# Kernel optimization log

Hardware: AMD Instinct MI355X
Metric: run time of the kernel (lower is better)

## Reference

```python
import jax, jax.numpy as jnp
import numpy as np

HEADS, BS, HALO = 8, 8, 3
WIN = BS + 2 * HALO  # 14


def setup_inputs() -> dict:
    key = jax.random.key(0)
    k1, k2, k3, k4 = jax.random.split(key, 4)
    B, C, H, W = 16, 256, 64, 64
    dim_out_qk, dim_out_v = 256, 256
    std = C ** (-0.5)
    x = jax.random.normal(k1, (B, C, H, W), jnp.float32)
    Wq = jax.random.normal(k2, (dim_out_qk, C), jnp.float32) * std
    Wkv = jax.random.normal(k3, (dim_out_qk + dim_out_v, C), jnp.float32) * std
    pos_bias = jax.random.normal(k4, (HEADS, BS * BS, WIN * WIN), jnp.float32) * 0.02
    return {"x": x, "Wq": Wq, "Wkv": Wkv, "pos_bias": pos_bias}


def reference(x, Wq, Wkv, pos_bias):
    B, C, H, W = x.shape
    dhqk = Wq.shape[0] // HEADS            # 32
    dhv = Wkv.shape[0] // HEADS - dhqk     # 32
    scale = dhqk ** (-0.5)
    nhb, nwb = H // BS, W // BS
    nb = nhb * nwb

    xl = jnp.transpose(x, (0, 2, 3, 1))    # [B, H, W, C]

    # queries: [B, heads, nb, bs^2, dhqk] (row-major within block)
    q = xl @ Wq.T
    q = q.reshape(B, nhb, BS, nwb, BS, HEADS, dhqk)
    q = q.transpose(0, 5, 1, 3, 2, 4, 6).reshape(B, HEADS, nb, BS * BS, dhqk)

    # keys/values via overlapping halo windows (zero-padded unfold)
    kv = xl @ Wkv.T                                       # [B, H, W, dim_kv]
    kv = jnp.pad(kv, ((0, 0), (HALO, HALO), (HALO, HALO), (0, 0)))
    ridx = (jnp.arange(nhb) * BS)[:, None] + jnp.arange(WIN)[None, :]
    cidx = (jnp.arange(nwb) * BS)[:, None] + jnp.arange(WIN)[None, :]
    kv = kv[:, ridx]
    kv = kv[:, :, :, cidx]
    kv = kv.transpose(0, 1, 3, 2, 4, 5).reshape(B, nb, WIN * WIN, HEADS, dhqk + dhv)
    k = kv[..., :dhqk]
    v = kv[..., dhqk:]

    attn = jnp.einsum('bhnqd,bnkhd->bhnqk', q, k) * scale + pos_bias[None, :, None]
    attn = jax.nn.softmax(attn, axis=-1)
    out = jnp.einsum('bhnqk,bnkhd->bhnqd', attn, v)       # [B, heads, nb, bs^2, dhv]

    out = out.reshape(B, HEADS, nhb, nwb, BS, BS, dhv)
    out = out.transpose(0, 1, 6, 2, 4, 3, 5).reshape(B, HEADS * dhv, H, W)
    return out
```

## Files before the change

kernel.cpp:

```cpp
#include <hip/hip_runtime.h>
#include <hip/hip_bf16.h>
#include <stdint.h>

#define HEADS 8
#define WIN 14
#define NPOS 196
#define NPAD 224
#define NB 16
#define NC 256
#define NH 64
#define NW 64
#define NP 4096
#define NKV 512
#define NOC 768

typedef __bf16 bf16_t;
typedef bf16_t bf16x8 __attribute__((ext_vector_type(8)));
typedef float f32x4 __attribute__((ext_vector_type(4)));

union Frag {
  uint4 u4;
  bf16x8 b8;
  ushort us[8];
};

__device__ __forceinline__ ushort f2bf(float f) {
  bf16_t h = (bf16_t)f;
  return __builtin_bit_cast(ushort, h);
}
__device__ __forceinline__ bf16x8 load_bf8(const float* __restrict__ p) {
  float4 a = *reinterpret_cast<const float4*>(p);
  float4 b = *reinterpret_cast<const float4*>(p + 4);
  bf16x8 r;
  r[0] = (bf16_t)a.x; r[1] = (bf16_t)a.y; r[2] = (bf16_t)a.z; r[3] = (bf16_t)a.w;
  r[4] = (bf16_t)b.x; r[5] = (bf16_t)b.y; r[6] = (bf16_t)b.z; r[7] = (bf16_t)b.w;
  return r;
}

__device__ ushort g_wb[NOC * NC];

__global__ __launch_bounds__(256) void k_wcast(const float* __restrict__ wq,
                                               const float* __restrict__ wkv) {
  int idx = (blockIdx.x * 256 + threadIdx.x) * 8;
  int oc = idx >> 8, c = idx & 255;
  const float* src = (oc < 256) ? (wq + (size_t)oc * NC + c)
                                : (wkv + (size_t)(oc - 256) * NC + c);
  Frag v;
  v.b8 = load_bf8(src);
  *reinterpret_cast<uint4*>(g_wb + idx) = v.u4;
}

__global__ __launch_bounds__(256) void k_xt(const float* __restrict__ x,
                                            ushort* __restrict__ xt) {
  __shared__ __align__(16) ushort ls[64][66];
  const int b = blockIdx.z, p0 = blockIdx.x * 64, c0 = blockIdx.y * 64;
  const int tid = threadIdx.x;
  #pragma unroll
  for (int it = 0; it < 4; ++it) {
    int i = it * 256 + tid;
    int c = i >> 4, ps = (i & 15) * 4;
    float4 v = *reinterpret_cast<const float4*>(x + ((size_t)(b * NC + c0 + c)) * NP + p0 + ps);
    ls[ps + 0][c] = f2bf(v.x);
    ls[ps + 1][c] = f2bf(v.y);
    ls[ps + 2][c] = f2bf(v.z);
    ls[ps + 3][c] = f2bf(v.w);
  }
  __syncthreads();
  #pragma unroll
  for (int it = 0; it < 2; ++it) {
    int i = it * 256 + tid;
    int p = i >> 3, cs = (i & 7) * 8;
    Frag o;
    #pragma unroll
    for (int j = 0; j < 8; ++j) o.us[j] = ls[p][cs + j];
    *reinterpret_cast<uint4*>(xt + ((size_t)(b * NP) + p0 + p) * NC + c0 + cs) = o.u4;
  }
}

__global__ __launch_bounds__(256, 2) void k_proj2(const ushort* __restrict__ xt,
                                                  ushort* __restrict__ qkv) {
  __shared__ __align__(16) ushort As[128][264];
  const int row0 = blockIdx.x * 128;
  const int n0 = blockIdx.y * 256;
  const int tid = threadIdx.x, lane = tid & 63, wid = tid >> 6;
  const int quad = lane >> 4, lc = lane & 15;
  #pragma unroll
  for (int it = 0; it < 16; ++it) {
    int i = it * 256 + tid;
    int r = i >> 5, cs = (i & 31) * 8;
    uint4 v = *reinterpret_cast<const uint4*>(xt + ((size_t)(row0 + r)) * NC + cs);
    *reinterpret_cast<uint4*>(&As[r][cs]) = v;
  }
  __syncthreads();
  const int wm = (wid & 1) * 64, wn = (wid >> 1) * 128;
  f32x4 acc[4][8] = {};
  #pragma unroll
  for (int ks = 0; ks < 8; ++ks) {
    const int k0 = ks * 32 + quad * 8;
    Frag a[4];
    #pragma unroll
    for (int mt = 0; mt < 4; ++mt)
      a[mt].u4 = *reinterpret_cast<const uint4*>(&As[wm + mt * 16 + lc][k0]);
    #pragma unroll
    for (int ng = 0; ng < 2; ++ng) {
      Frag bb[4];
      #pragma unroll
      for (int j = 0; j < 4; ++j) {
        int oc = n0 + wn + (ng * 4 + j) * 16 + lc;
        bb[j].u4 = *reinterpret_cast<const uint4*>(g_wb + (size_t)oc * NC + k0);
      }
      #pragma unroll
      for (int mt = 0; mt < 4; ++mt)
        #pragma unroll
        for (int j = 0; j < 4; ++j)
          acc[mt][ng * 4 + j] = __builtin_amdgcn_mfma_f32_16x16x32_bf16(
              a[mt].b8, bb[j].b8, acc[mt][ng * 4 + j], 0, 0, 0);
    }
  }
  __syncthreads();
  #pragma unroll
  for (int mt = 0; mt < 4; ++mt)
    #pragma unroll
    for (int nn = 0; nn < 8; ++nn)
      #pragma unroll
      for (int r = 0; r < 4; ++r)
        As[wm + mt * 16 + quad * 4 + r][wn + nn * 16 + lc] = f2bf(acc[mt][nn][r]);
  __syncthreads();
  #pragma unroll
  for (int it = 0; it < 16; ++it) {
    int i = it * 256 + tid;
    int r = i >> 5, cs = (i & 31) * 8;
    uint4 u = *reinterpret_cast<const uint4*>(&As[r][cs]);
    *reinterpret_cast<uint4*>(qkv + ((size_t)(row0 + r)) * NOC + n0 + cs) = u;
  }
}

__global__ __launch_bounds__(256) void k_attn_f2(const ushort* __restrict__ qkv,
                                                 const float* __restrict__ pbias,
                                                 float* __restrict__ out) {
  __shared__ __align__(16) ushort ksh[NPAD][40];
  __shared__ __align__(16) ushort vth[32][232];
  __shared__ __align__(16) ushort psh[4][16][32];
  float (*osh)[33] = reinterpret_cast<float(*)[33]>(&ksh[0][0]);
  const int b = blockIdx.z, h = blockIdx.y, blk = blockIdx.x;
  const int by = blk >> 3, bx = blk & 7;
  const int tid = threadIdx.x, lane = tid & 63, w = tid >> 6;
  const int quad = lane >> 4, lc = lane & 15;

  Frag aq;
  {
    int q = w * 16 + lc;
    int py = by * 8 + (q >> 3), px = bx * 8 + (q & 7);
    aq.u4 = *reinterpret_cast<const uint4*>(
        qkv + ((size_t)(b * NP + py * NW + px)) * NOC + h * 32 + quad * 8);
  }

  for (int it = 0; it < 7; ++it) {
    int i = it * 256 + tid;
    int pos = i >> 3, seg = i & 7;
    Frag v;
    v.u4 = make_uint4(0u, 0u, 0u, 0u);
    if (pos < NPOS) {
      int wy = pos / WIN;
      int wx = pos - wy * WIN;
      int yq = by * 8 - 3 + wy, xx = bx * 8 - 3 + wx;
      if ((unsigned)yq < (unsigned)NH && (unsigned)xx < (unsigned)NW)
        v.u4 = *reinterpret_cast<const uint4*>(
            qkv + ((size_t)(b * NP + yq * NW + xx)) * NOC + 256 + h * 64 + seg * 8);
    }
    if (seg < 4) {
      *reinterpret_cast<uint4*>(&ksh[pos][seg * 8]) = v.u4;
    } else {
      int d0 = (seg - 4) * 8;
      int cp = pos ^ ((seg - 4) << 3);
      #pragma unroll
      for (int j = 0; j < 8; ++j) vth[d0 + j][cp] = v.us[j];
    }
  }
  __syncthreads();

  f32x4 s[14];
  #pragma unroll
  for (int nt = 0; nt < 14; ++nt) {
    Frag bk;
    bk.u4 = *reinterpret_cast<const uint4*>(&ksh[nt * 16 + lc][quad * 8]);
    f32x4 z = {0.f, 0.f, 0.f, 0.f};
    s[nt] = __builtin_amdgcn_mfma_f32_16x16x32_bf16(aq.b8, bk.b8, z, 0, 0, 0);
  }

  const float scale = 0.17677669529663687f;
  const int qi = w * 16 + quad * 4;
  float lsum[4] = {0.f, 0.f, 0.f, 0.f};
  #pragma unroll
  for (int nt = 0; nt < 14; ++nt) {
    int col = nt * 16 + lc;
    #pragma unroll
    for (int r = 0; r < 4; ++r) {
      float p = 0.f;
      if (col < NPOS)
        p = __expf(s[nt][r] * scale + pbias[(size_t)(h * 64 + qi + r) * NPOS + col]);
      s[nt][r] = p;
      lsum[r] += p;
    }
  }

  f32x4 o[2] = {};
  #pragma unroll
  for (int kt = 0; kt < 7; ++kt) {
    #pragma unroll
    for (int t = 0; t < 2; ++t)
      #pragma unroll
      for (int r = 0; r < 4; ++r)
        psh[w][quad * 4 + r][t * 16 + lc] = f2bf(s[2 * kt + t][r]);
    Frag ap;
    ap.u4 = *reinterpret_cast<const uint4*>(&psh[w][lc][quad * 8]);
    #pragma unroll
    for (int t = 0; t < 2; ++t) {
      int d = t * 16 + lc;
      int g = (kt * 4 + quad) ^ ((d >> 3) & 3);
      Frag bv;
      bv.u4 = *reinterpret_cast<const uint4*>(&vth[d][g * 8]);
      o[t] = __builtin_amdgcn_mfma_f32_16x16x32_bf16(ap.b8, bv.b8, o[t], 0, 0, 0);
    }
  }

  #pragma unroll
  for (int m = 1; m < 16; m <<= 1)
    #pragma unroll
    for (int r = 0; r < 4; ++r) lsum[r] += __shfl_xor(lsum[r], m);
  float rinv[4];
  #pragma unroll
  for (int r = 0; r < 4; ++r) rinv[r] = 1.0f / lsum[r];

  __syncthreads();
  #pragma unroll
  for (int t = 0; t < 2; ++t)
    #pragma unroll
    for (int r = 0; r < 4; ++r)
      osh[w * 16 + quad * 4 + r][t * 16 + lc] = o[t][r] * rinv[r];
  __syncthreads();

  {
    int d = tid >> 3, yy = tid & 7;
    float4 o0, o1;
    o0.x = osh[yy * 8 + 0][d]; o0.y = osh[yy * 8 + 1][d];
    o0.z = osh[yy * 8 + 2][d]; o0.w = osh[yy * 8 + 3][d];
    o1.x = osh[yy * 8 + 4][d]; o1.y = osh[yy * 8 + 5][d];
    o1.z = osh[yy * 8 + 6][d]; o1.w = osh[yy * 8 + 7][d];
    float* op = out + ((size_t)(b * NC + h * 32 + d) * NH + by * 8 + yy) * NW + bx * 8;
    *reinterpret_cast<float4*>(op) = o0;
    *reinterpret_cast<float4*>(op + 4) = o1;
  }
}

__global__ __launch_bounds__(256) void k_proj_r4(const float* __restrict__ x,
                                                 const float* __restrict__ wq,
                                                 const float* __restrict__ wkv,
                                                 ushort* __restrict__ qkv) {
  __shared__ __align__(16) ushort As[64][264];
  const int b = blockIdx.z, y = blockIdx.x;
  const int n0 = blockIdx.y * 256;
  const int tid = threadIdx.x, lane = tid & 63, wid = tid >> 6;
  const int quad = lane >> 4, lc = lane & 15;
  #pragma unroll
  for (int it = 0; it < 16; ++it) {
    int i = it * 256 + tid;
    int c = i >> 4, xs = (i & 15) * 4;
    float4 v = *reinterpret_cast<const float4*>(x + ((size_t)(b * NC + c)) * NP + y * NW + xs);
    #pragma unroll
    for (int j = 0; j < 4; ++j) {
      int row = xs + j;
      float f = (j == 0) ? v.x : (j == 1) ? v.y : (j == 2) ? v.z : v.w;
      As[row][c ^ ((((row >> 2) & 3)) << 3)] = f2bf(f);
    }
  }
  __syncthreads();
  const int wm = (wid & 1) * 32, wn = (wid >> 1) * 128;
  const int swz = ((lc >> 2) & 3) << 3;
  f32x4 acc[2][8] = {};
  #pragma unroll
  for (int ks = 0; ks < 8; ++ks) {
    const int k0 = ks * 32 + quad * 8;
    Frag a0, a1;
    a0.u4 = *reinterpret_cast<const uint4*>(&As[wm + lc][k0 ^ swz]);
    a1.u4 = *reinterpret_cast<const uint4*>(&As[wm + 16 + lc][k0 ^ swz]);
    #pragma unroll
    for (int nh = 0; nh < 2; ++nh) {
      bf16x8 bb[4];
      #pragma unroll
      for (int nt = 0; nt < 4; ++nt) {
        int oc = n0 + wn + nh * 64 + nt * 16 + lc;
        const float* wp = (oc < 256) ? (wq + (size_t)oc * NC) : (wkv + (size_t)(oc - 256) * NC);
        bb[nt] = load_bf8(wp + k0);
      }
      #pragma unroll
      for (int nt = 0; nt < 4; ++nt) {
        acc[0][nh * 4 + nt] = __builtin_amdgcn_mfma_f32_16x16x32_bf16(a0.b8, bb[nt], acc[0][nh * 4 + nt], 0, 0, 0);
        acc[1][nh * 4 + nt] = __builtin_amdgcn_mfma_f32_16x16x32_bf16(a1.b8, bb[nt], acc[1][nh * 4 + nt], 0, 0, 0);
      }
    }
  }
  __syncthreads();
  #pragma unroll
  for (int mt = 0; mt < 2; ++mt)
    #pragma unroll
    for (int nn = 0; nn < 8; ++nn)
      #pragma unroll
      for (int r = 0; r < 4; ++r)
        As[wm + mt * 16 + quad * 4 + r][wn + nn * 16 + lc] = f2bf(acc[mt][nn][r]);
  __syncthreads();
  #pragma unroll
  for (int v8 = 0; v8 < 8; ++v8) {
    int flat = v8 * 256 + tid;
    int p = flat >> 5, seg = flat & 31;
    uint4 u = *reinterpret_cast<const uint4*>(&As[p][seg * 8]);
    *reinterpret_cast<uint4*>(qkv + ((size_t)(b * NP) + y * NW + p) * NOC + n0 + seg * 8) = u;
  }
}

__global__ __launch_bounds__(256) void k_kv(const float* __restrict__ x,
                                            const float* __restrict__ wkv,
                                            ushort* __restrict__ kvb) {
  __shared__ __align__(16) ushort As[64][264];
  const int b = blockIdx.z;
  const int y = blockIdx.x;
  const int n0 = blockIdx.y * 128;
  const int tid = threadIdx.x;
  const int lane = tid & 63, wid = tid >> 6;
  const int quad = lane >> 4, lc = lane & 15;
  #pragma unroll
  for (int it = 0; it < 16; ++it) {
    int i = it * 256 + tid;
    int c = i >> 4, xs = (i & 15) * 4;
    float4 v = *reinterpret_cast<const float4*>(x + ((size_t)(b * NC + c)) * NP + y * NW + xs);
    As[xs + 0][c] = f2bf(v.x);
    As[xs + 1][c] = f2bf(v.y);
    As[xs + 2][c] = f2bf(v.z);
    As[xs + 3][c] = f2bf(v.w);
  }
  __syncthreads();
  const int wm = (wid & 1) * 32, wn = (wid >> 1) * 64;
  f32x4 acc[2][4] = {};
  #pragma unroll
  for (int ks = 0; ks < 8; ++ks) {
    const int k0 = ks * 32 + quad * 8;
    Frag a[2];
    bf16x8 bb[4];
    #pragma unroll
    for (int mt = 0; mt < 2; ++mt)
      a[mt].u4 = *reinterpret_cast<const uint4*>(&As[wm + mt * 16 + lc][k0]);
    #pragma unroll
    for (int nt = 0; nt < 4; ++nt) {
      int oc = n0 + wn + nt * 16 + lc;
      bb[nt] = load_bf8(wkv + (size_t)oc * NC + k0);
    }
    #pragma unroll
    for (int mt = 0; mt < 2; ++mt)
      #pragma unroll
      for (int nt = 0; nt < 4; ++nt)
        acc[mt][nt] = __builtin_amdgcn_mfma_f32_16x16x32_bf16(a[mt].b8, bb[nt], acc[mt][nt], 0, 0, 0);
  }
  #pragma unroll
  for (int mt = 0; mt < 2; ++mt) {
    #pragma unroll
    for (int r = 0; r < 4; ++r) {
      int pl = wm + mt * 16 + quad * 4 + r;
      #pragma unroll
      for (int nt = 0; nt < 4; ++nt) {
        int oc = n0 + wn + nt * 16 + lc;
        kvb[((size_t)(b * NP + y * NW + pl)) * NKV + oc] = f2bf(acc[mt][nt][r]);
      }
    }
  }
}

__global__ __launch_bounds__(256) void k_attn_v3(const float* __restrict__ x,
                                                 const float* __restrict__ wq,
                                                 const ushort* __restrict__ kvb,
                                                 const float* __restrict__ pbias,
                                                 float* __restrict__ out) {
  __shared__ __align__(16) ushort ksh[NPAD][40];
  __shared__ __align__(16) ushort vth[32][232];
  __shared__ __align__(16) ushort psh[4][16][232];
  __shared__ __align__(16) ushort qsh[4][16][32];
  __shared__ __align__(16) float osh[64][33];
  const int b = blockIdx.z, h = blockIdx.y, blk = blockIdx.x;
  const int by = blk >> 3, bx = blk & 7;
  const int tid = threadIdx.x, lane = tid & 63, w = tid >> 6;
  const int quad = lane >> 4, lc = lane & 15;

  for (int it = 0; it < 7; ++it) {
    int i = it * 256 + tid;
    int pos = i >> 3, seg = i & 7;
    Frag v;
    v.u4 = make_uint4(0u, 0u, 0u, 0u);
    if (pos < NPOS) {
      int wy = pos / WIN;
      int wx = pos - wy * WIN;
      int yq = by * 8 - 3 + wy, xx = bx * 8 - 3 + wx;
      if ((unsigned)yq < (unsigned)NH && (unsigned)xx < (unsigned)NW)
        v.u4 = *reinterpret_cast<const uint4*>(
            kvb + ((size_t)(b * NP + yq * NW + xx)) * NKV + h * 64 + seg * 8);
    }
    if (seg < 4) {
      *reinterpret_cast<uint4*>(&ksh[pos][seg * 8]) = v.u4;
    } else {
      int d0 = (seg - 4) * 8;
      #pragma unroll
      for (int j = 0; j < 8; ++j) vth[d0 + j][pos] = v.us[j];
    }
  }

  f32x4 qacc[2] = {};
  {
    const int q = w * 16 + lc;
    const size_t p = (size_t)(by * 8 + (q >> 3)) * NW + bx * 8 + (q & 7);
    #pragma unroll
    for (int ks = 0; ks < 8; ++ks) {
      const int k0 = ks * 32 + quad * 8;
      Frag ax;
      #pragma unroll
      for (int j = 0; j < 8; ++j)
        ax.us[j] = f2bf(x[((size_t)(b * NC + k0 + j)) * NP + p]);
      bf16x8 bw0 = load_bf8(wq + (size_t)(h * 32 + lc) * NC + k0);
      bf16x8 bw1 = load_bf8(wq + (size_t)(h * 32 + 16 + lc) * NC + k0);
      qacc[0] = __builtin_amdgcn_mfma_f32_16x16x32_bf16(ax.b8, bw0, qacc[0], 0, 0, 0);
      qacc[1] = __builtin_amdgcn_mfma_f32_16x16x32_bf16(ax.b8, bw1, qacc[1], 0, 0, 0);
    }
  }
  #pragma unroll
  for (int t = 0; t < 2; ++t)
    #pragma unroll
    for (int r = 0; r < 4; ++r)
      qsh[w][quad * 4 + r][t * 16 + lc] = f2bf(qacc[t][r]);
  Frag aq;
  aq.u4 = *reinterpret_cast<const uint4*>(&qsh[w][lc][quad * 8]);

  __syncthreads();

  f32x4 s[14];
  #pragma unroll
  for (int nt = 0; nt < 14; ++nt) {
    Frag bk;
    bk.u4 = *reinterpret_cast<const uint4*>(&ksh[nt * 16 + lc][quad * 8]);
    f32x4 z = {0.f, 0.f, 0.f, 0.f};
    s[nt] = __builtin_amdgcn_mfma_f32_16x16x32_bf16(aq.b8, bk.b8, z, 0, 0, 0);
  }

  const float scale = 0.17677669529663687f;
  const int qi = w * 16 + quad * 4;
  float lsum[4] = {0.f, 0.f, 0.f, 0.f};
  #pragma unroll
  for (int nt = 0; nt < 14; ++nt) {
    int col = nt * 16 + lc;
    #pragma unroll
    for (int r = 0; r < 4; ++r) {
      float p = 0.f;
      if (col < NPOS)
        p = __expf(s[nt][r] * scale + pbias[(size_t)(h * 64 + qi + r) * NPOS + col]);
      s[nt][r] = p;
      lsum[r] += p;
    }
  }
  #pragma unroll
  for (int m = 1; m < 16; m <<= 1) {
    #pragma unroll
    for (int r = 0; r < 4; ++r) lsum[r] += __shfl_xor(lsum[r], m);
  }
  #pragma unroll
  for (int nt = 0; nt < 14; ++nt) {
    #pragma unroll
    for (int r = 0; r < 4; ++r) psh[w][quad * 4 + r][nt * 16 + lc] = f2bf(s[nt][r]);
  }
  f32x4 o[2] = {};
  #pragma unroll
  for (int kt = 0; kt < 7; ++kt) {
    Frag ap;
    ap.u4 = *reinterpret_cast<const uint4*>(&psh[w][lc][kt * 32 + quad * 8]);
    #pragma unroll
    for (int t = 0; t < 2; ++t) {
      Frag bv;
      bv.u4 = *reinterpret_cast<const uint4*>(&vth[t * 16 + lc][kt * 32 + quad * 8]);
      o[t] = __builtin_amdgcn_mfma_f32_16x16x32_bf16(ap.b8, bv.b8, o[t], 0, 0, 0);
    }
  }
  #pragma unroll
  for (int t = 0; t < 2; ++t)
    #pragma unroll
    for (int r = 0; r < 4; ++r)
      osh[w * 16 + quad * 4 + r][t * 16 + lc] = o[t][r] / lsum[r];
  __syncthreads();
  {
    int d = tid >> 3, yy = tid & 7;
    float4 o0, o1;
    o0.x = osh[yy * 8 + 0][d]; o0.y = osh[yy * 8 + 1][d];
    o0.z = osh[yy * 8 + 2][d]; o0.w = osh[yy * 8 + 3][d];
    o1.x = osh[yy * 8 + 4][d]; o1.y = osh[yy * 8 + 5][d];
    o1.z = osh[yy * 8 + 6][d]; o1.w = osh[yy * 8 + 7][d];
    float* op = out + ((size_t)(b * NC + h * 32 + d) * NH + by * 8 + yy) * NW + bx * 8;
    *reinterpret_cast<float4*>(op) = o0;
    *reinterpret_cast<float4*>(op + 4) = o1;
  }
}

extern "C" void kernel_launch(void* const* d_in, const int* in_sizes, int n_in,
                              void* d_out, int out_size, void* d_ws, size_t ws_size,
                              hipStream_t stream) {
  const float* x   = (const float*)d_in[0];
  const float* wq  = (const float*)d_in[1];
  const float* wkv = (const float*)d_in[2];
  const float* pb  = (const float*)d_in[3];
  float* outp = (float*)d_out;

  const size_t qkv_bytes = (size_t)NB * NP * NOC * sizeof(ushort);
  const size_t xt_bytes  = (size_t)NB * NP * NC * sizeof(ushort);

  if (ws_size >= qkv_bytes + xt_bytes) {
    ushort* qkv = (ushort*)d_ws;
    ushort* xt  = (ushort*)((char*)d_ws + qkv_bytes);
    k_wcast<<<dim3(NOC * NC / (256 * 8)), 256, 0, stream>>>(wq, wkv);
    k_xt<<<dim3(NP / 64, NC / 64, NB), 256, 0, stream>>>(x, xt);
    k_proj2<<<dim3(NB * NP / 128, 3), 256, 0, stream>>>(xt, qkv);
    k_attn_f2<<<dim3(64, HEADS, NB), 256, 0, stream>>>(qkv, pb, outp);
  } else if (ws_size >= qkv_bytes) {
    ushort* qkv = (ushort*)d_ws;
    k_proj_r4<<<dim3(NH, 3, NB), 256, 0, stream>>>(x, wq, wkv, qkv);
    k_attn_f2<<<dim3(64, HEADS, NB), 256, 0, stream>>>(qkv, pb, outp);
  } else {
    ushort* kvb = (ushort*)d_ws;
    k_kv<<<dim3(NH, NKV / 128, NB), 256, 0, stream>>>(x, wkv, kvb);
    k_attn_v3<<<dim3(64, HEADS, NB), 256, 0, stream>>>(x, wq, kvb, pb, outp);
  }
}
```

Before: 291.4 us.

## Swizzle xt layout for direct global-to-LDS loads and pre-transpose position bias

k_xt now writes xt with an XOR-swizzled 8-element group order, so k_proj2 can copy its A tile straight into LDS with global_load_lds and read it back conflict-free through the same XOR swizzle. The padded LDS row is dropped, and the epilogue staging uses the swizzle too. A new k_pbt kernel transposes pos_bias once per call into a [head][key][query] layout padded with large negative values, so the attention kernel loads four biases with one float4 and no column bounds check. The cost is an extra small kernel launch and a tighter coupling of the xt layout between the two kernels.

```diff
diff --git a/kernel.cpp b/kernel.cpp
--- a/kernel.cpp
+++ b/kernel.cpp
@@ -37,7 +37,18 @@
   return r;
 }
 
+__device__ __forceinline__ void gload_lds16(const ushort* g, ushort* l) {
+#if __has_builtin(__builtin_amdgcn_global_load_lds)
+  __builtin_amdgcn_global_load_lds(
+      (const __attribute__((address_space(1))) unsigned int*)(const void*)g,
+      (__attribute__((address_space(3))) unsigned int*)(void*)l, 16, 0, 0);
+#else
+  *reinterpret_cast<uint4*>(l) = *reinterpret_cast<const uint4*>(g);
+#endif
+}
+
 __device__ ushort g_wb[NOC * NC];
+__device__ float g_pbt[HEADS * NPAD * 64];
 
 __global__ __launch_bounds__(256) void k_wcast(const float* __restrict__ wq,
                                                const float* __restrict__ wkv) {
@@ -50,10 +61,20 @@
   *reinterpret_cast<uint4*>(g_wb + idx) = v.u4;
 }
 
+__global__ __launch_bounds__(256) void k_pbt(const float* __restrict__ pb) {
+  const int h = blockIdx.y;
+  const int key = blockIdx.x * 4 + (threadIdx.x >> 6);
+  const int q = threadIdx.x & 63;
+  float v = -30000.0f;
+  if (key < NPOS) v = pb[((size_t)(h * 64 + q)) * NPOS + key];
+  g_pbt[((size_t)(h * NPAD) + key) * 64 + q] = v;
+}
+
 __global__ __launch_bounds__(256) void k_xt(const float* __restrict__ x,
                                             ushort* __restrict__ xt) {
   __shared__ __align__(16) ushort ls[64][66];
   const int b = blockIdx.z, p0 = blockIdx.x * 64, c0 = blockIdx.y * 64;
+  const int by8 = blockIdx.y * 8;
   const int tid = threadIdx.x;
   #pragma unroll
   for (int it = 0; it < 4; ++it) {
@@ -69,27 +90,27 @@
   #pragma unroll
   for (int it = 0; it < 2; ++it) {
     int i = it * 256 + tid;
-    int p = i >> 3, cs = (i & 7) * 8;
+    int p = i >> 3, gl = i & 7;
     Frag o;
     #pragma unroll
-    for (int j = 0; j < 8; ++j) o.us[j] = ls[p][cs + j];
-    *reinterpret_cast<uint4*>(xt + ((size_t)(b * NP) + p0 + p) * NC + c0 + cs) = o.u4;
+    for (int j = 0; j < 8; ++j) o.us[j] = ls[p][gl * 8 + j];
+    int gph = by8 + (gl ^ (p & 7));
+    *reinterpret_cast<uint4*>(xt + ((size_t)(b * NP) + p0 + p) * NC + gph * 8) = o.u4;
   }
 }
 
 __global__ __launch_bounds__(256, 2) void k_proj2(const ushort* __restrict__ xt,
                                                   ushort* __restrict__ qkv) {
-  __shared__ __align__(16) ushort As[128][264];
+  __shared__ __align__(16) ushort As[128 * 256];
   const int row0 = blockIdx.x * 128;
   const int n0 = blockIdx.y * 256;
   const int tid = threadIdx.x, lane = tid & 63, wid = tid >> 6;
   const int quad = lane >> 4, lc = lane & 15;
+  const ushort* gs = xt + (size_t)row0 * NC;
   #pragma unroll
   for (int it = 0; it < 16; ++it) {
-    int i = it * 256 + tid;
-    int r = i >> 5, cs = (i & 31) * 8;
-    uint4 v = *reinterpret_cast<const uint4*>(xt + ((size_t)(row0 + r)) * NC + cs);
-    *reinterpret_cast<uint4*>(&As[r][cs]) = v;
+    int f = it * 256 + tid;
+    gload_lds16(gs + (size_t)f * 8, As + f * 8);
   }
   __syncthreads();
   const int wm = (wid & 1) * 64, wn = (wid >> 1) * 128;
@@ -99,8 +120,11 @@
     const int k0 = ks * 32 + quad * 8;
     Frag a[4];
     #pragma unroll
-    for (int mt = 0; mt < 4; ++mt)
-      a[mt].u4 = *reinterpret_cast<const uint4*>(&As[wm + mt * 16 + lc][k0]);
+    for (int mt = 0; mt < 4; ++mt) {
+      int row = wm + mt * 16 + lc;
+      int gk = (ks * 4 + quad) ^ (lc & 7);
+      a[mt].u4 = *reinterpret_cast<const uint4*>(&As[row * 256 + gk * 8]);
+    }
     #pragma unroll
     for (int ng = 0; ng < 2; ++ng) {
       Frag bb[4];
@@ -121,22 +145,26 @@
   #pragma unroll
   for (int mt = 0; mt < 4; ++mt)
     #pragma unroll
-    for (int nn = 0; nn < 8; ++nn)
-      #pragma unroll
-      for (int r = 0; r < 4; ++r)
-        As[wm + mt * 16 + quad * 4 + r][wn + nn * 16 + lc] = f2bf(acc[mt][nn][r]);
+    for (int nn = 0; nn < 8; ++nn) {
+      int row = wm + mt * 16 + quad * 4;
+      #pragma unroll
+      for (int r = 0; r < 4; ++r) {
+        int rr = row + r;
+        int col = wn + nn * 16 + lc;
+        As[rr * 256 + (((col >> 3) ^ (rr & 7)) * 8) + (col & 7)] = f2bf(acc[mt][nn][r]);
+      }
+    }
   __syncthreads();
   #pragma unroll
   for (int it = 0; it < 16; ++it) {
     int i = it * 256 + tid;
-    int r = i >> 5, cs = (i & 31) * 8;
-    uint4 u = *reinterpret_cast<const uint4*>(&As[r][cs]);
-    *reinterpret_cast<uint4*>(qkv + ((size_t)(row0 + r)) * NOC + n0 + cs) = u;
+    int r = i >> 5, g = i & 31;
+    uint4 u = *reinterpret_cast<const uint4*>(&As[r * 256 + ((g ^ (r & 7)) * 8)]);
+    *reinterpret_cast<uint4*>(qkv + ((size_t)(row0 + r)) * NOC + n0 + g * 8) = u;
   }
 }
 
 __global__ __launch_bounds__(256) void k_attn_f2(const ushort* __restrict__ qkv,
-                                                 const float* __restrict__ pbias,
                                                  float* __restrict__ out) {
   __shared__ __align__(16) ushort ksh[NPAD][40];
   __shared__ __align__(16) ushort vth[32][232];
@@ -190,15 +218,15 @@
 
   const float scale = 0.17677669529663687f;
   const int qi = w * 16 + quad * 4;
+  const float* __restrict__ pbh = g_pbt + (size_t)h * (NPAD * 64);
   float lsum[4] = {0.f, 0.f, 0.f, 0.f};
   #pragma unroll
   for (int nt = 0; nt < 14; ++nt) {
     int col = nt * 16 + lc;
+    float4 bv = *reinterpret_cast<const float4*>(pbh + col * 64 + qi);
     #pragma unroll
     for (int r = 0; r < 4; ++r) {
-      float p = 0.f;
-      if (col < NPOS)
-        p = __expf(s[nt][r] * scale + pbias[(size_t)(h * 64 + qi + r) * NPOS + col]);
+      float p = __expf(s[nt][r] * scale + (&bv.x)[r]);
       s[nt][r] = p;
       lsum[r] += p;
     }
@@ -519,13 +547,15 @@
     ushort* qkv = (ushort*)d_ws;
     ushort* xt  = (ushort*)((char*)d_ws + qkv_bytes);
     k_wcast<<<dim3(NOC * NC / (256 * 8)), 256, 0, stream>>>(wq, wkv);
+    k_pbt<<<dim3(NPAD / 4, HEADS), 256, 0, stream>>>(pb);
     k_xt<<<dim3(NP / 64, NC / 64, NB), 256, 0, stream>>>(x, xt);
     k_proj2<<<dim3(NB * NP / 128, 3), 256, 0, stream>>>(xt, qkv);
-    k_attn_f2<<<dim3(64, HEADS, NB), 256, 0, stream>>>(qkv, pb, outp);
+    k_attn_f2<<<dim3(64, HEADS, NB), 256, 0, stream>>>(qkv, outp);
   } else if (ws_size >= qkv_bytes) {
     ushort* qkv = (ushort*)d_ws;
+    k_pbt<<<dim3(NPAD / 4, HEADS), 256, 0, stream>>>(pb);
     k_proj_r4<<<dim3(NH, 3, NB), 256, 0, stream>>>(x, wq, wkv, qkv);
-    k_attn_f2<<<dim3(64, HEADS, NB), 256, 0, stream>>>(qkv, pb, outp);
+    k_attn_f2<<<dim3(64, HEADS, NB), 256, 0, stream>>>(qkv, outp);
   } else {
     ushort* kvb = (ushort*)d_ws;
     k_kv<<<dim3(NH, NKV / 128, NB), 256, 0, stream>>>(x, wkv, kvb);
```

New measurement: 303.2 us. 4.0% more time.
